# Performance work log

Measured on AMD Instinct MI355X. Metric: run time of the kernel, lower is better.

Reference implementation:

```python
import jax, jax.numpy as jnp
import numpy as np

B, S, N, F, H = 128, 128, 24, 16, 32  # batch, seq, nodes, in-feat/node, hid/node


def setup_inputs() -> dict:
    key = jax.random.key(0)
    ks = jax.random.split(key, 7)
    IS, HS = N * F, N * H
    stdv = 1.0 / np.sqrt(HS).astype(np.float32)
    x = jax.random.normal(ks[0], (B, S, N, F), jnp.float32)
    h0 = jax.random.normal(ks[1], (B, N, H), jnp.float32)
    c0 = jax.random.normal(ks[2], (B, N, H), jnp.float32)
    G = jax.random.normal(ks[3], (N, N), jnp.float32)
    W = jax.random.uniform(ks[4], (IS, 4 * HS), jnp.float32, -stdv, stdv)
    U = jax.random.uniform(ks[5], (HS, 4 * HS), jnp.float32, -stdv, stdv)
    bias = jax.random.uniform(ks[6], (4 * HS,), jnp.float32, -stdv, stdv)
    return {"x": x, "h0": h0, "c0": c0, "W": W, "U": U, "bias": bias, "G": G}


def _graph_masks(G, F, H):
    # repeat_interleave(G, r, dim=-2) == kron(G, ones(r,1)); dim=-1 == kron(G, ones(1,c)).
    # Then tile x4 along last dim for the 4 LSTM gates.
    GW = jnp.tile(jnp.kron(G, jnp.ones((F, H), G.dtype)), (1, 4))  # [N*F, 4*N*H]
    GU = jnp.tile(jnp.kron(G, jnp.ones((H, H), G.dtype)), (1, 4))  # [N*H, 4*N*H]
    return GW, GU


def reference(x, h0, c0, W, U, bias, G):
    B, S, N, F = x.shape
    H = h0.shape[-1]
    HS = N * H
    GW, GU = _graph_masks(G, F, H)
    Wm = W * GW                      # masked input weights
    Um = U * GU                      # masked recurrent weights
    # Non-recurrent term batched into one big GEMM over all timesteps.
    xf = x.reshape(B, S, N * F)
    xg = jnp.einsum('bsi,ig->bsg', xf, Wm) + bias  # [B,S,4*HS]
    h = h0.reshape(B, HS)
    c = c0.reshape(B, HS)

    def step(carry, xg_t):
        h, c = carry
        gates = xg_t + h @ Um
        i = jax.nn.sigmoid(gates[:, :HS])
        f = jax.nn.sigmoid(gates[:, HS:2 * HS])
        g = jnp.tanh(gates[:, 2 * HS:3 * HS])
        o = jax.nn.sigmoid(gates[:, 3 * HS:])
        c = f * c + i * g
        h = o * jnp.tanh(c)
        return (h, c), h

    (h, c), hs = jax.lax.scan(step, (h, c), jnp.swapaxes(xg, 0, 1))  # hs: [S,B,HS]
    hidden_seq = jnp.swapaxes(hs, 0, 1).reshape(B, S, N, H)
    return hidden_seq, (h.reshape(B, N, H), c.reshape(B, N, H))
```

## Files before the change

### kernel.cpp

```cpp
#include <hip/hip_runtime.h>
#include <hip/hip_bf16.h>


typedef __bf16 bf16x8 __attribute__((ext_vector_type(8)));
typedef float f32x4 __attribute__((ext_vector_type(4)));

#define HS 768
#define GATES 3072
#define KV 1152
#define SEQ 128
#define BATCH 128
#define OUT_HID (BATCH*SEQ*HS)
#define BPITCH 1160

__device__ __forceinline__ float fast_sig(float x) {
    return 1.0f / (1.0f + __expf(-x));
}
__device__ __forceinline__ float fast_tanh(float x) {
    x = fminf(fmaxf(x, -15.0f), 15.0f);
    float e = __expf(2.0f * x);
    return (e - 1.0f) / (e + 1.0f);
}

__device__ __forceinline__ bf16x8 cvt8(const float* src) {
    float4 v0 = *(const float4*)src;
    float4 v1 = *(const float4*)(src + 4);
    bf16x8 p;
    p[0] = (__bf16)v0.x; p[1] = (__bf16)v0.y; p[2] = (__bf16)v0.z; p[3] = (__bf16)v0.w;
    p[4] = (__bf16)v1.x; p[5] = (__bf16)v1.y; p[6] = (__bf16)v1.z; p[7] = (__bf16)v1.w;
    return p;
}

__device__ __forceinline__ int swz(int c8, int row) {
    return (c8 & ~3) | ((c8 & 3) ^ (row & 3));
}

__global__ void prep_kernel(const float* __restrict__ W, const float* __restrict__ U,
                            const float* __restrict__ G, __bf16* __restrict__ VmT) {
    __shared__ __bf16 tile[64][65];
    const int kvb = blockIdx.x * 64;
    const int cb  = blockIdx.y * 64;
    const int tid = threadIdx.x;
    {
        const int cl = tid & 63, kl0 = tid >> 6;
        #pragma unroll
        for (int i = 0; i < 16; ++i) {
            int kl = kl0 + i * 4;
            int kv = kvb + kl;
            int c  = cb + cl;
            int nout = (c % HS) >> 5;
            float g, v;
            if (kv < 384) {
                g = G[(kv >> 4) * 24 + nout];
                v = W[(size_t)kv * GATES + c];
            } else {
                int ku = kv - 384;
                g = G[(ku >> 5) * 24 + nout];
                v = U[(size_t)ku * GATES + c];
            }
            tile[kl][cl] = (__bf16)(v * g);
        }
    }
    __syncthreads();
    {
        const int kl = tid & 63, cl0 = tid >> 6;
        #pragma unroll
        for (int i = 0; i < 16; ++i) {
            int c = cl0 + i * 4;
            VmT[(size_t)(cb + c) * KV + kvb + kl] = tile[kl][c];
        }
    }
}

__global__ void prep_x(const float* __restrict__ x, __bf16* __restrict__ xb) {
    const int g = blockIdx.x * 256 + threadIdx.x;
    const int e = g * 8;
    const int b = e / (SEQ * 384);
    const int rem = e - b * (SEQ * 384);
    const int t = rem / 384;
    const int k = rem - t * 384;
    *(bf16x8*)&xb[((size_t)t * BATCH + b) * 384 + k] = cvt8(&x[e]);
}

__global__ __launch_bounds__(256, 1) void scan_kernel(
        const __bf16* __restrict__ xb,
        const float* __restrict__ h0,
        const float* __restrict__ c0,
        const __bf16* __restrict__ VmT,
        const float* __restrict__ bias,
        float* out,
        unsigned* xh32,
        unsigned* bar) {
    __shared__ __align__(16) __bf16 Bs[16 * BPITCH];
    const int tid = threadIdx.x;
    const int lane = tid & 63, wv = tid >> 6;
    const int m = lane & 15, quad = lane >> 4;
    const int team = blockIdx.x & 7, wg = blockIdx.x >> 3;
    const int bbase = team * 16;
    const int jbase = wg * 32 + wv * 8;

    bf16x8 w[2][36];
    #pragma unroll
    for (int T = 0; T < 2; ++T) {
        const int cg = (m & 3) * HS + jbase + 2 * (m >> 2) + T;
        const __bf16* wp = VmT + (size_t)cg * KV;
        #pragma unroll
        for (int kk = 0; kk < 36; ++kk)
            w[T][kk] = *(const bf16x8*)(wp + kk * 32 + quad * 8);
    }

    const int b_own = bbase + m;
    const int j0 = jbase + 2 * quad;
    const int j1 = j0 + 1;
    float cv0 = c0[b_own * HS + j0];
    float cv1 = c0[b_own * HS + j1];
    f32x4 bias0, bias1;
    #pragma unroll
    for (int r = 0; r < 4; ++r) {
        bias0[r] = bias[r * HS + j0];
        bias1[r] = bias[r * HS + j1];
    }

    unsigned* cnt = bar + team * 64;
    const int bq = (quad ^ (m & 3));

    #pragma unroll
    for (int i = 0; i < 3; ++i) {
        int ch = tid + i * 256;
        int row = ch / 48, c8 = ch % 48;
        *(uint4*)&Bs[row * BPITCH + swz(c8, row) * 8] =
            *(const uint4*)&xb[((size_t)0 * BATCH + bbase + row) * 384 + c8 * 8];
    }
    #pragma unroll
    for (int i = 0; i < 6; ++i) {
        int ch = tid + i * 256;
        int row = ch / 96, c8h = ch % 96;
        bf16x8 p = cvt8(&h0[(size_t)(bbase + row) * HS + c8h * 8]);
        *(bf16x8*)&Bs[row * BPITCH + (48 + swz(c8h, row)) * 8] = p;
    }
    __syncthreads();

    #pragma unroll 1
    for (int t = 0; t < SEQ; ++t) {
        f32x4 acc0 = bias0, acc1 = bias1;
        #pragma unroll
        for (int kk = 0; kk < 36; ++kk) {
            bf16x8 bf = *(const bf16x8*)&Bs[m * BPITCH + kk * 32 + bq * 8];
            acc0 = __builtin_amdgcn_mfma_f32_16x16x32_bf16(w[0][kk], bf, acc0, 0, 0, 0);
            acc1 = __builtin_amdgcn_mfma_f32_16x16x32_bf16(w[1][kk], bf, acc1, 0, 0, 0);
        }

        float h0v, h1v;
        {
            float ii = fast_sig(acc0[0]), ff = fast_sig(acc0[1]);
            float gg = fast_tanh(acc0[2]), oo = fast_sig(acc0[3]);
            cv0 = ff * cv0 + ii * gg;
            h0v = oo * fast_tanh(cv0);
        }
        {
            float ii = fast_sig(acc1[0]), ff = fast_sig(acc1[1]);
            float gg = fast_tanh(acc1[2]), oo = fast_sig(acc1[3]);
            cv1 = ff * cv1 + ii * gg;
            h1v = oo * fast_tanh(cv1);
        }

        const size_t obase = ((size_t)b_own * SEQ + t) * HS;
        out[obase + j0] = h0v;
        out[obase + j1] = h1v;

        if (t == SEQ - 1) {
            out[OUT_HID + b_own * HS + j0] = h0v;
            out[OUT_HID + b_own * HS + j1] = h1v;
            out[OUT_HID + BATCH * HS + b_own * HS + j0] = cv0;
            out[OUT_HID + BATCH * HS + b_own * HS + j1] = cv1;
            break;
        }

        {
            unsigned lo = (unsigned)__builtin_bit_cast(unsigned short, (__bf16)h0v);
            unsigned hi = (unsigned)__builtin_bit_cast(unsigned short, (__bf16)h1v);
            unsigned* dst = xh32 + ((size_t)(t & 1) * BATCH + b_own) * 384
                                 + (jbase >> 1) + quad;
            (void)__hip_atomic_exchange(dst, lo | (hi << 16), __ATOMIC_RELAXED,
                                        __HIP_MEMORY_SCOPE_AGENT);
        }

        __syncthreads();

        #pragma unroll
        for (int i = 0; i < 3; ++i) {
            int ch = tid + i * 256;
            int row = ch / 48, c8 = ch % 48;
            *(uint4*)&Bs[row * BPITCH + swz(c8, row) * 8] =
                *(const uint4*)&xb[((size_t)(t + 1) * BATCH + bbase + row) * 384 + c8 * 8];
        }

        if (tid == 0) {
            __hip_atomic_fetch_add(cnt, 1u, __ATOMIC_RELAXED,
                                   __HIP_MEMORY_SCOPE_AGENT);
            while (__hip_atomic_load(cnt, __ATOMIC_RELAXED,
                                     __HIP_MEMORY_SCOPE_AGENT) < (unsigned)(24 * (t + 1))) {
                __builtin_amdgcn_s_sleep(1);
            }
        }
        __syncthreads();

        {
            const unsigned* src = xh32 + (size_t)(t & 1) * BATCH * 384;
            unsigned vals[24];
            #pragma unroll
            for (int i = 0; i < 24; ++i) {
                int ch = tid + i * 256;
                int row = ch / 384, u = ch % 384;
                vals[i] = __hip_atomic_load(&src[(size_t)(bbase + row) * 384 + u],
                                            __ATOMIC_RELAXED, __HIP_MEMORY_SCOPE_AGENT);
            }
            #pragma unroll
            for (int i = 0; i < 24; ++i) {
                int ch = tid + i * 256;
                int row = ch / 384, u = ch % 384;
                int c8h = u >> 2;
                int eo = (u & 3) * 2;
                *(unsigned*)&Bs[row * BPITCH + (48 + swz(c8h, row)) * 8 + eo] = vals[i];
            }
        }
        __syncthreads();
    }
}

extern "C" void kernel_launch(void* const* d_in, const int* in_sizes, int n_in,
                              void* d_out, int out_size, void* d_ws, size_t ws_size,
                              hipStream_t stream) {
    (void)in_sizes; (void)n_in; (void)out_size; (void)ws_size;
    const float* x    = (const float*)d_in[0];
    const float* h0   = (const float*)d_in[1];
    const float* c0   = (const float*)d_in[2];
    const float* W    = (const float*)d_in[3];
    const float* U    = (const float*)d_in[4];
    const float* bias = (const float*)d_in[5];
    const float* G    = (const float*)d_in[6];
    float* out = (float*)d_out;

    char* wsb = (char*)d_ws;
    unsigned* bar = (unsigned*)wsb;
    __bf16* VmT  = (__bf16*)(wsb + 4096);
    __bf16* xb   = (__bf16*)(wsb + 4096 + (size_t)GATES * KV * 2);
    unsigned* xh32 = (unsigned*)(wsb + 4096 + (size_t)GATES * KV * 2
                                      + (size_t)SEQ * BATCH * 384 * 2);

    hipMemsetAsync(bar, 0, 4096, stream);
    prep_kernel<<<dim3(18, 48), 256, 0, stream>>>(W, U, G, VmT);
    prep_x<<<dim3(3072), 256, 0, stream>>>(x, xb);
    scan_kernel<<<dim3(192), dim3(256), 0, stream>>>(xb, h0, c0, VmT, bias,
                                                     out, xh32, bar);
}
```

Baseline: 640.2 us.

## Replace counter barrier with per-element step-tagged h exchange and polling

```diff
diff --git a/kernel.cpp b/kernel.cpp
--- a/kernel.cpp
+++ b/kernel.cpp
@@ -12,6 +12,8 @@
 #define BATCH 128
 #define OUT_HID (BATCH*SEQ*HS)
 #define BPITCH 1160
+#define NWG 192
+#define XH_BYTES ((size_t)2 * BATCH * 384 * 8)
 
 __device__ __forceinline__ float fast_sig(float x) {
     return 1.0f / (1.0f + __expf(-x));
@@ -89,8 +91,7 @@
         const __bf16* __restrict__ VmT,
         const float* __restrict__ bias,
         float* out,
-        unsigned* xh32,
-        unsigned* bar) {
+        unsigned long long* xh64) {
     __shared__ __align__(16) __bf16 Bs[16 * BPITCH];
     const int tid = threadIdx.x;
     const int lane = tid & 63, wv = tid >> 6;
@@ -121,7 +122,6 @@
         bias1[r] = bias[r * HS + j1];
     }
 
-    unsigned* cnt = bar + team * 64;
     const int bq = (quad ^ (m & 3));
 
     #pragma unroll
@@ -164,11 +164,10 @@
             h1v = oo * fast_tanh(cv1);
         }
 
-        const size_t obase = ((size_t)b_own * SEQ + t) * HS;
-        out[obase + j0] = h0v;
-        out[obase + j1] = h1v;
-
         if (t == SEQ - 1) {
+            const size_t obase = ((size_t)b_own * SEQ + t) * HS;
+            out[obase + j0] = h0v;
+            out[obase + j1] = h1v;
             out[OUT_HID + b_own * HS + j0] = h0v;
             out[OUT_HID + b_own * HS + j1] = h1v;
             out[OUT_HID + BATCH * HS + b_own * HS + j0] = cv0;
@@ -179,13 +178,29 @@
         {
             unsigned lo = (unsigned)__builtin_bit_cast(unsigned short, (__bf16)h0v);
             unsigned hi = (unsigned)__builtin_bit_cast(unsigned short, (__bf16)h1v);
-            unsigned* dst = xh32 + ((size_t)(t & 1) * BATCH + b_own) * 384
-                                 + (jbase >> 1) + quad;
-            (void)__hip_atomic_exchange(dst, lo | (hi << 16), __ATOMIC_RELAXED,
-                                        __HIP_MEMORY_SCOPE_AGENT);
+            unsigned long long pk = ((unsigned long long)(unsigned)(t + 1) << 32)
+                                  | (unsigned long long)(lo | (hi << 16));
+            unsigned long long* dst = xh64 + ((size_t)(t & 1) * BATCH + b_own) * 384
+                                           + (jbase >> 1) + quad;
+            __hip_atomic_store(dst, pk, __ATOMIC_RELAXED, __HIP_MEMORY_SCOPE_AGENT);
+        }
+        {
+            const size_t obase = ((size_t)b_own * SEQ + t) * HS;
+            out[obase + j0] = h0v;
+            out[obase + j1] = h1v;
         }
 
         __syncthreads();
+
+        const unsigned long long* src64 = xh64 + (size_t)(t & 1) * BATCH * 384;
+        unsigned long long v64[24];
+        #pragma unroll
+        for (int i = 0; i < 24; ++i) {
+            int ch = tid + i * 256;
+            int row = ch / 384, u = ch % 384;
+            v64[i] = __hip_atomic_load(&src64[(size_t)(bbase + row) * 384 + u],
+                                       __ATOMIC_RELAXED, __HIP_MEMORY_SCOPE_AGENT);
+        }
 
         #pragma unroll
         for (int i = 0; i < 3; ++i) {
@@ -195,34 +210,35 @@
                 *(const uint4*)&xb[((size_t)(t + 1) * BATCH + bbase + row) * 384 + c8 * 8];
         }
 
-        if (tid == 0) {
-            __hip_atomic_fetch_add(cnt, 1u, __ATOMIC_RELAXED,
-                                   __HIP_MEMORY_SCOPE_AGENT);
-            while (__hip_atomic_load(cnt, __ATOMIC_RELAXED,
-                                     __HIP_MEMORY_SCOPE_AGENT) < (unsigned)(24 * (t + 1))) {
-                __builtin_amdgcn_s_sleep(1);
+        {
+            const unsigned tag = (unsigned)(t + 1);
+            for (;;) {
+                bool any = false;
+                #pragma unroll
+                for (int i = 0; i < 24; ++i)
+                    if ((unsigned)(v64[i] >> 32) != tag) any = true;
+                if (!any) break;
+                #pragma unroll
+                for (int i = 0; i < 24; ++i) {
+                    if ((unsigned)(v64[i] >> 32) != tag) {
+                        int ch = tid + i * 256;
+                        int row = ch / 384, u = ch % 384;
+                        v64[i] = __hip_atomic_load(
+                            &src64[(size_t)(bbase + row) * 384 + u],
+                            __ATOMIC_RELAXED, __HIP_MEMORY_SCOPE_AGENT);
+                    }
+                }
             }
         }
-        __syncthreads();
-
-        {
-            const unsigned* src = xh32 + (size_t)(t & 1) * BATCH * 384;
-            unsigned vals[24];
-            #pragma unroll
-            for (int i = 0; i < 24; ++i) {
-                int ch = tid + i * 256;
-                int row = ch / 384, u = ch % 384;
-                vals[i] = __hip_atomic_load(&src[(size_t)(bbase + row) * 384 + u],
-                                            __ATOMIC_RELAXED, __HIP_MEMORY_SCOPE_AGENT);
-            }
-            #pragma unroll
-            for (int i = 0; i < 24; ++i) {
-                int ch = tid + i * 256;
-                int row = ch / 384, u = ch % 384;
-                int c8h = u >> 2;
-                int eo = (u & 3) * 2;
-                *(unsigned*)&Bs[row * BPITCH + (48 + swz(c8h, row)) * 8 + eo] = vals[i];
-            }
+
+        #pragma unroll
+        for (int i = 0; i < 24; ++i) {
+            int ch = tid + i * 256;
+            int row = ch / 384, u = ch % 384;
+            int c8h = u >> 2;
+            int eo = (u & 3) * 2;
+            *(unsigned*)&Bs[row * BPITCH + (48 + swz(c8h, row)) * 8 + eo] =
+                (unsigned)v64[i];
         }
         __syncthreads();
     }
@@ -242,15 +258,13 @@
     float* out = (float*)d_out;
 
     char* wsb = (char*)d_ws;
-    unsigned* bar = (unsigned*)wsb;
-    __bf16* VmT  = (__bf16*)(wsb + 4096);
-    __bf16* xb   = (__bf16*)(wsb + 4096 + (size_t)GATES * KV * 2);
-    unsigned* xh32 = (unsigned*)(wsb + 4096 + (size_t)GATES * KV * 2
-                                      + (size_t)SEQ * BATCH * 384 * 2);
-
-    hipMemsetAsync(bar, 0, 4096, stream);
+    unsigned long long* xh64 = (unsigned long long*)wsb;
+    __bf16* VmT = (__bf16*)(wsb + XH_BYTES);
+    __bf16* xb  = (__bf16*)(wsb + XH_BYTES + (size_t)GATES * KV * 2);
+
+    hipMemsetAsync(xh64, 0, XH_BYTES, stream);
     prep_kernel<<<dim3(18, 48), 256, 0, stream>>>(W, U, G, VmT);
     prep_x<<<dim3(3072), 256, 0, stream>>>(x, xb);
-    scan_kernel<<<dim3(192), dim3(256), 0, stream>>>(xb, h0, c0, VmT, bias,
-                                                     out, xh32, bar);
-}
+    scan_kernel<<<dim3(NWG), dim3(256), 0, stream>>>(xb, h0, c0, VmT, bias,
+                                                     out, xh64);
+}
```

New measurement: 1.186 ms. +85.2%, slower.
